# Performance work log

Measured on AMD Instinct MI355X. Metric: run time of the kernel, lower is better.

Reference implementation:

```python
import jax, jax.numpy as jnp
import numpy as np

L, D_MODEL, D_INNER, DT_RANK, D_STATE, D_CONV, VOCAB = 4, 768, 1536, 48, 16, 4, 32000
B, S = 1, 1024


def rmsnorm(x, w, eps=1e-5):
    return x * jax.lax.rsqrt(jnp.mean(x * x, axis=-1, keepdims=True) + eps) * w


def causal_depthwise_conv(x, w, b):
    # x: [B,S,D]; w: [D,1,K] (torch Conv1d groups=D weight layout); causal left-pad K-1
    y = jax.lax.conv_general_dilated(
        x.transpose(0, 2, 1), w, window_strides=(1,), padding=[(D_CONV - 1, 0)],
        dimension_numbers=('NCH', 'OIH', 'NCH'), feature_group_count=D_INNER)
    return y.transpose(0, 2, 1) + b


def selective_scan(u, dt, A, Bm, Cm, Dv):
    # Faithful to the source: A_delta = exp(dt (x) A), clamp(min=-20) is a no-op on exp output
    A_delta = jnp.clip(jnp.exp(jnp.einsum('bld,dn->bldn', dt, A)), -20.0, None)
    B_delta_u = jnp.einsum('bld,bld,bln->bldn', dt, u, Bm)
    shifted = jnp.pad(A_delta[:, 1:], ((0, 0), (1, 0), (0, 0), (0, 0)))
    A_cum = jnp.exp(jnp.cumsum(shifted, axis=1))
    h = B_delta_u / (A_cum + 1e-12)
    y = jnp.einsum('bldn,bln->bld', jnp.cumsum(h, axis=1) * A_cum, Cm)
    return y + u * Dv


def setup_inputs() -> dict:
    key = jax.random.key(0)
    ks = jax.random.split(key, 8)
    return {
        'tokens': jax.random.randint(ks[0], (B, S), 0, VOCAB),
        'embedding': jax.random.normal(ks[1], (VOCAB, D_MODEL), jnp.float32) * 0.02,
        'norm_w': jnp.ones((L, D_MODEL), jnp.float32),
        'in_proj_w': jax.random.normal(ks[2], (L, 2 * D_INNER, D_MODEL), jnp.float32) * 0.02,
        'conv_w': jax.random.normal(ks[3], (L, D_INNER, 1, D_CONV), jnp.float32) * 0.2,
        'conv_b': jnp.zeros((L, D_INNER), jnp.float32),
        'x_proj_w': jax.random.normal(ks[4], (L, DT_RANK + 2 * D_STATE, D_INNER), jnp.float32) * 0.02,
        'dt_proj_w': jax.random.normal(ks[5], (L, D_INNER, DT_RANK), jnp.float32) * 0.001,
        'dt_proj_b': jnp.full((L, D_INNER), 5.0, jnp.float32),  # delta~5 keeps exp(cumsum(exp(dt*A))) finite
        'A_log': jnp.tile(jnp.log(jnp.arange(1, D_STATE + 1, dtype=jnp.float32)), (L, D_INNER, 1)),
        'D_skip': jnp.ones((L, D_INNER), jnp.float32),
        'out_proj_w': jax.random.normal(ks[6], (L, D_MODEL, D_INNER), jnp.float32) * 0.02,
        'final_norm_w': jnp.ones((D_MODEL,), jnp.float32),
    }


def reference(tokens, embedding, norm_w, in_proj_w, conv_w, conv_b, x_proj_w,
              dt_proj_w, dt_proj_b, A_log, D_skip, out_proj_w, final_norm_w):
    x = embedding[tokens]  # [B,S,d_model]
    for i in range(L):
        h = rmsnorm(x, norm_w[i])
        xz = h @ in_proj_w[i].T                      # [B,S,2*d_inner]
        xi, res = xz[..., :D_INNER], xz[..., D_INNER:]
        xi = jax.nn.silu(causal_depthwise_conv(xi, conv_w[i], conv_b[i]))
        proj = xi @ x_proj_w[i].T                    # [B,S,dt_rank+2*d_state]
        dt = jax.nn.softplus(proj[..., :DT_RANK] @ dt_proj_w[i].T + dt_proj_b[i])
        Bm = proj[..., DT_RANK:DT_RANK + D_STATE]
        Cm = proj[..., DT_RANK + D_STATE:]
        A = -jnp.exp(A_log[i])                       # [d_inner, d_state]
        y = selective_scan(xi, dt, A, Bm, Cm, D_skip[i])
        x = x + (y * jax.nn.silu(res)) @ out_proj_w[i].T
    return rmsnorm(x, final_norm_w) @ embedding.T    # tied LM head: [B,S,vocab]
```

## Files before the change

kernel.cpp:

```cpp
#include <hip/hip_runtime.h>
#include <hip/hip_bf16.h>
#include <cmath>

namespace {

constexpr int kL      = 4;
constexpr int kDModel = 768;
constexpr int kDInner = 1536;
constexpr int kDtRank = 48;
constexpr int kDState = 16;
constexpr int kDConv  = 4;
constexpr int kSeq    = 1024;
constexpr int kPLd    = 96;
constexpr int kPB     = 128;
constexpr int kVocab  = 32000;
constexpr int kCH     = 64;
constexpr int kNCH    = kSeq / kCH;
constexpr int kDN     = kDInner * kDState;

using short8 = __attribute__((ext_vector_type(8))) short;
using f32x4  = __attribute__((ext_vector_type(4))) float;

__device__ __forceinline__ float silu_f(float v) {
    return v / (1.f + __expf(-v));
}

__device__ __forceinline__ void split_bf16(float v, __hip_bfloat16& hi, __hip_bfloat16& lo) {
    hi = __float2bfloat16(v);
    lo = __float2bfloat16(v - __bfloat162float(hi));
}

__global__ void __launch_bounds__(256) f2b_kernel(
    const float* __restrict__ src, __hip_bfloat16* __restrict__ dst, int n) {
    int i = (blockIdx.x * 256 + threadIdx.x) * 4;
    const int stride = gridDim.x * 256 * 4;
    for (; i + 3 < n; i += stride) {
        const float4 v = *reinterpret_cast<const float4*>(src + i);
        dst[i + 0] = __float2bfloat16(v.x);
        dst[i + 1] = __float2bfloat16(v.y);
        dst[i + 2] = __float2bfloat16(v.z);
        dst[i + 3] = __float2bfloat16(v.w);
    }
}

__global__ void __launch_bounds__(256) split3_kernel(
    const float* __restrict__ src, int ldsrc, int rows, int cols,
    __hip_bfloat16* __restrict__ dst, int rowsPad) {
    const int idx = blockIdx.x * 256 + threadIdx.x;
    if (idx >= rowsPad * cols) return;
    const int r = idx / cols, c = idx % cols;
    const float v = (r < rows) ? src[(size_t)r * ldsrc + c] : 0.f;
    __hip_bfloat16 hi, lo;
    split_bf16(v, hi, lo);
    __hip_bfloat16* row = dst + (size_t)r * 3 * cols;
    row[c] = hi; row[cols + c] = hi; row[2 * cols + c] = lo;
}

__global__ void __launch_bounds__(256) embed_kernel(
    const int* __restrict__ tokens, const float* __restrict__ emb,
    float* __restrict__ x) {
    const int s = blockIdx.x;
    const int t = tokens[s];
    const float* src = emb + (size_t)t * kDModel;
    float* dst = x + (size_t)s * kDModel;
    for (int d = threadIdx.x; d < kDModel; d += blockDim.x) dst[d] = src[d];
}

template <bool SPLIT>
__global__ void __launch_bounds__(256) rmsnorm_kernel(
    const float* __restrict__ x, const float* __restrict__ w,
    __hip_bfloat16* __restrict__ out) {
    const int s = blockIdx.x;
    const float* row = x + (size_t)s * kDModel;
    float ss = 0.f;
    for (int d = threadIdx.x; d < kDModel; d += blockDim.x) {
        const float v = row[d];
        ss = fmaf(v, v, ss);
    }
    #pragma unroll
    for (int m = 32; m; m >>= 1) ss += __shfl_xor(ss, m);
    __shared__ float red[4];
    if ((threadIdx.x & 63) == 0) red[threadIdx.x >> 6] = ss;
    __syncthreads();
    const float total = red[0] + red[1] + red[2] + red[3];
    const float scale = rsqrtf(total / (float)kDModel + 1e-5f);
    __hip_bfloat16* dst = out + (size_t)s * (SPLIT ? 3 * kDModel : kDModel);
    for (int d = threadIdx.x; d < kDModel; d += blockDim.x) {
        const float v = row[d] * scale * w[d];
        if (SPLIT) {
            __hip_bfloat16 hi, lo;
            split_bf16(v, hi, lo);
            dst[d] = hi; dst[kDModel + d] = lo; dst[2 * kDModel + d] = hi;
        } else {
            dst[d] = __float2bfloat16(v);
        }
    }
}

template <int BM, int BN, int KSPLIT>
__global__ void __launch_bounds__((BN == 256) ? 512 : 256) mfma_gemm(
    const __hip_bfloat16* __restrict__ A, int lda,
    const __hip_bfloat16* __restrict__ B, int ldb,
    float* __restrict__ C, int ldc,
    int N, int K, size_t partStride) {
    constexpr int BK = 32;
    constexpr int THREADS = (BN == 256) ? 512 : 256;
    constexpr int WAVES_M = 2;
    constexpr int WAVES_N = THREADS / 64 / WAVES_M;
    constexpr int LPT = (BM * 4 + BN * 4) / THREADS;
    static_assert(BM == 128, "A staging assumes BM=128");
    __shared__ unsigned short As[2][BM * BK];
    __shared__ unsigned short Bs[2][BN * BK];
    const int tid  = threadIdx.x;
    const int lane = tid & 63;

    const int nwg = gridDim.x * gridDim.y;
    int bid = blockIdx.y * gridDim.x + blockIdx.x;
    {
        const int q = nwg >> 3, r = nwg & 7;
        const int xcd = bid & 7, pos = bid >> 3;
        bid = (xcd < r ? xcd * (q + 1) : r * (q + 1) + (xcd - r) * q) + pos;
    }
    const int m0 = (bid % gridDim.x) * BM;
    const int n0 = (bid / gridDim.x) * BN;

    const int Kp = K / KSPLIT;
    const int kbeg = (KSPLIT > 1) ? blockIdx.z * Kp : 0;
    float* Cw = (KSPLIT > 1) ? C + (size_t)blockIdx.z * partStride : C;
    constexpr int WM = BM / WAVES_M, WN = BN / WAVES_N;
    constexpr int MR = WM / 16, NR = WN / 16;
    const int wave = tid >> 6;
    const int wm = (wave / WAVES_N) * WM, wn = (wave % WAVES_N) * WN;
    const int l15 = lane & 15, l4 = lane >> 4;
    f32x4 acc[MR][NR] = {};

    auto stage = [&](int buf, int k0) {
        #pragma unroll
        for (int i = 0; i < BM * 4 / THREADS; ++i) {
            const int idx = tid + i * THREADS;
            const int r = idx >> 2, qv = idx & 3;
            const int qs = qv ^ ((r >> 1) & 3);
            __builtin_amdgcn_global_load_lds(
                (const __attribute__((address_space(1))) void*)(A + (size_t)(m0 + r) * lda + k0 + qs * 8),
                (__attribute__((address_space(3))) void*)(&As[buf][(idx - lane) * 8]),
                16, 0, 0);
        }
        #pragma unroll
        for (int i = 0; i < BN * 4 / THREADS; ++i) {
            const int idx = tid + i * THREADS;
            const int r = idx >> 2, qv = idx & 3;
            const int qs = qv ^ ((r >> 1) & 3);
            __builtin_amdgcn_global_load_lds(
                (const __attribute__((address_space(1))) void*)(B + (size_t)(n0 + r) * ldb + k0 + qs * 8),
                (__attribute__((address_space(3))) void*)(&Bs[buf][(idx - lane) * 8]),
                16, 0, 0);
        }
    };

    const int nt = Kp / BK;
    int cur = 0;
    stage(0, kbeg);
    for (int t = 0; t < nt; ++t) {
        if (t + 1 < nt) {
            stage(cur ^ 1, kbeg + (t + 1) * BK);
            if constexpr (LPT == 4) asm volatile("s_waitcnt vmcnt(4)" ::: "memory");
            else                    asm volatile("s_waitcnt vmcnt(3)" ::: "memory");
        } else {
            asm volatile("s_waitcnt vmcnt(0)" ::: "memory");
        }
        __builtin_amdgcn_s_barrier();

        short8 af[MR], bfv[NR];
        #pragma unroll
        for (int mi = 0; mi < MR; ++mi) {
            const int R = wm + mi * 16 + l15;
            af[mi] = *reinterpret_cast<const short8*>(&As[cur][(R * 4 + (l4 ^ ((R >> 1) & 3))) * 8]);
        }
        #pragma unroll
        for (int ni = 0; ni < NR; ++ni) {
            const int R = wn + ni * 16 + l15;
            bfv[ni] = *reinterpret_cast<const short8*>(&Bs[cur][(R * 4 + (l4 ^ ((R >> 1) & 3))) * 8]);
        }
        #pragma unroll
        for (int mi = 0; mi < MR; ++mi)
            #pragma unroll
            for (int ni = 0; ni < NR; ++ni)
                acc[mi][ni] = __builtin_amdgcn_mfma_f32_16x16x32_bf16(
                    af[mi], bfv[ni], acc[mi][ni], 0, 0, 0);

        asm volatile("s_waitcnt lgkmcnt(0)" ::: "memory");
        __builtin_amdgcn_s_barrier();
        cur ^= 1;
    }

    #pragma unroll
    for (int mi = 0; mi < MR; ++mi) {
        const int mrow = m0 + wm + mi * 16 + l4 * 4;
        #pragma unroll
        for (int ni = 0; ni < NR; ++ni) {
            const int ncol = n0 + wn + ni * 16 + l15;
            if (ncol >= N) continue;
            #pragma unroll
            for (int r = 0; r < 4; ++r)
                Cw[(size_t)(mrow + r) * ldc + ncol] = acc[mi][ni][r];
        }
    }
}

template <int NP, bool ADD>
__global__ void __launch_bounds__(256) reduce_parts(
    const float* __restrict__ parts, size_t stride,
    float* __restrict__ dst, int count) {
    const int i = (blockIdx.x * 256 + threadIdx.x) * 4;
    if (i >= count) return;
    float4 s = *reinterpret_cast<const float4*>(parts + i);
    #pragma unroll
    for (int p = 1; p < NP; ++p) {
        const float4 v = *reinterpret_cast<const float4*>(parts + (size_t)p * stride + i);
        s.x += v.x; s.y += v.y; s.z += v.z; s.w += v.w;
    }
    float4* d = reinterpret_cast<float4*>(dst + i);
    if (ADD) {
        float4 o = *d;
        o.x += s.x; o.y += s.y; o.z += s.z; o.w += s.w;
        *d = o;
    } else {
        *d = s;
    }
}

__global__ void __launch_bounds__(256) dt_kernel(
    const float* __restrict__ proj, const float* __restrict__ dtw,
    const float* __restrict__ bias, float* __restrict__ dt) {
    __shared__ float sw[kDtRank][257];
    const int tid = threadIdx.x;
    const int n0 = blockIdx.x * 256;
    const int m0 = blockIdx.y * 8;
    for (int idx = tid; idx < 256 * kDtRank; idx += 256) {
        const int nn = idx / kDtRank, k = idx % kDtRank;
        sw[k][nn] = dtw[(size_t)(n0 + nn) * kDtRank + k];
    }
    __syncthreads();
    const int n = n0 + tid;
    const float b = bias[n];
    #pragma unroll
    for (int mi = 0; mi < 8; ++mi) {
        const float* pr = proj + (size_t)(m0 + mi) * kPLd;
        float acc = b;
        #pragma unroll
        for (int k = 0; k < kDtRank; ++k)
            acc = fmaf(pr[k], sw[k][tid], acc);
        acc = (acc > 20.f) ? acc : log1pf(__expf(acc));
        dt[(size_t)(m0 + mi) * kDInner + n] = acc;
    }
}

__global__ void __launch_bounds__(256) conv_silu_kernel(
    const float* __restrict__ p0, const float* __restrict__ p1,
    const float* __restrict__ cw, const float* __restrict__ cb,
    float* __restrict__ xi, __hip_bfloat16* __restrict__ xi2) {
    const int s = blockIdx.x;
    const int d = blockIdx.y * 256 + threadIdx.x;
    float acc = cb[d];
    #pragma unroll
    for (int k = 0; k < kDConv; ++k) {
        const int sl = s - (kDConv - 1) + k;
        if (sl >= 0) {
            const size_t off = (size_t)sl * (2 * kDInner) + d;
            acc = fmaf(p0[off] + p1[off], cw[d * kDConv + k], acc);
        }
    }
    const float v = silu_f(acc);
    xi[(size_t)s * kDInner + d] = v;
    __hip_bfloat16 hi, lo;
    split_bf16(v, hi, lo);
    __hip_bfloat16* row = xi2 + (size_t)s * 3 * kDInner;
    row[d] = hi; row[kDInner + d] = lo; row[2 * kDInner + d] = hi;
}

__global__ void __launch_bounds__(256) scan_part1(
    const float* __restrict__ dt, const float* __restrict__ u,
    const float* __restrict__ proj, const float* __restrict__ A_log,
    float* __restrict__ P, float* __restrict__ S) {
    __shared__ float sdt[kCH][16], su[kCH][16], sB[kCH][16];
    const int tid = threadIdx.x;
    const int n = tid & 15, dl = tid >> 4;
    const int d0 = blockIdx.x * 16;
    const int l0 = blockIdx.y * kCH;
    for (int idx = tid; idx < kCH * 16; idx += 256) {
        const int r = idx >> 4, c = idx & 15;
        sdt[r][c] = dt[(size_t)(l0 + r) * kDInner + d0 + c];
        su [r][c] = u [(size_t)(l0 + r) * kDInner + d0 + c];
        sB [r][c] = proj[(size_t)(l0 + r) * kPLd + kDtRank + c];
    }
    __syncthreads();
    const int d = d0 + dl;
    const float Adn = -__expf(A_log[d * kDState + n]);
    float state = 0.f, sumA = 0.f;
    #pragma unroll 8
    for (int l = 0; l < kCH; ++l) {
        const float dtv = sdt[l][dl];
        const float adelta = __expf(dtv * Adn);
        const float mult = __expf(adelta);
        state = fmaf(state, mult, dtv * su[l][dl] * sB[l][n]);
        sumA += adelta;
    }
    const int dn = d * kDState + n;
    P[(size_t)blockIdx.y * kDN + dn] = __expf(sumA);
    S[(size_t)blockIdx.y * kDN + dn] = state;
}

__global__ void __launch_bounds__(256) scan_part2(
    const float* __restrict__ dt, const float* __restrict__ u,
    const float* __restrict__ proj, const float* __restrict__ A_log,
    const float* __restrict__ D_skip, const float* __restrict__ P,
    const float* __restrict__ S, float* __restrict__ y) {
    __shared__ float sdt[kCH][16], su[kCH][16], sB[kCH][16], sC[kCH][16];
    __shared__ float sy[kCH][16];
    const int tid = threadIdx.x;
    const int n = tid & 15, dl = tid >> 4;
    const int d0 = blockIdx.x * 16;
    const int l0 = blockIdx.y * kCH;
    for (int idx = tid; idx < kCH * 16; idx += 256) {
        const int r = idx >> 4, c = idx & 15;
        sdt[r][c] = dt[(size_t)(l0 + r) * kDInner + d0 + c];
        su [r][c] = u [(size_t)(l0 + r) * kDInner + d0 + c];
        sB [r][c] = proj[(size_t)(l0 + r) * kPLd + kDtRank + c];
        sC [r][c] = proj[(size_t)(l0 + r) * kPLd + kDtRank + kDState + c];
    }
    const int dn = d0 * kDState + tid;
    float state = 0.f;
    for (int jj = 0; jj < (int)blockIdx.y; ++jj) {
        const size_t idx = (size_t)jj * kDN + dn;
        state = fmaf(state, P[idx], S[idx]);
    }
    __syncthreads();
    const int d = d0 + dl;
    const float Adn = -__expf(A_log[d * kDState + n]);
    const float Dv  = D_skip[d];
    for (int l = 0; l < kCH; ++l) {
        const float dtv = sdt[l][dl];
        const float uv  = su[l][dl];
        const float mult = __expf(__expf(dtv * Adn));
        state = fmaf(state, mult, dtv * uv * sB[l][n]);
        float contrib = state * sC[l][n];
        contrib += __shfl_xor(contrib, 8);
        contrib += __shfl_xor(contrib, 4);
        contrib += __shfl_xor(contrib, 2);
        contrib += __shfl_xor(contrib, 1);
        if (n == 0) sy[l][dl] = fmaf(uv, Dv, contrib);
    }
    __syncthreads();
    for (int idx = tid; idx < kCH * 16; idx += 256) {
        const int r = idx >> 4, c = idx & 15;
        y[(size_t)(l0 + r) * kDInner + d0 + c] = sy[r][c];
    }
}

__global__ void __launch_bounds__(256) mul_silu_kernel(
    const float* __restrict__ y, const float* __restrict__ p0,
    const float* __restrict__ p1, __hip_bfloat16* __restrict__ g2) {
    const int s = blockIdx.x;
    const int d = blockIdx.y * 256 + threadIdx.x;
    const size_t off = (size_t)s * (2 * kDInner) + kDInner + d;
    const float res = p0[off] + p1[off];
    const float v = y[(size_t)s * kDInner + d] * silu_f(res);
    __hip_bfloat16 hi, lo;
    split_bf16(v, hi, lo);
    __hip_bfloat16* row = g2 + (size_t)s * 3 * kDInner;
    row[d] = hi; row[kDInner + d] = lo; row[2 * kDInner + d] = hi;
}

}

extern "C" void kernel_launch(void* const* d_in, const int* in_sizes, int n_in,
                              void* d_out, int out_size, void* d_ws, size_t ws_size,
                              hipStream_t stream) {
    const int*   tokens       = (const int*)d_in[0];
    const float* embedding    = (const float*)d_in[1];
    const float* norm_w       = (const float*)d_in[2];
    const float* in_proj_w    = (const float*)d_in[3];
    const float* conv_w       = (const float*)d_in[4];
    const float* conv_b       = (const float*)d_in[5];
    const float* x_proj_w     = (const float*)d_in[6];
    const float* dt_proj_w    = (const float*)d_in[7];
    const float* dt_proj_b    = (const float*)d_in[8];
    const float* A_log        = (const float*)d_in[9];
    const float* D_skip       = (const float*)d_in[10];
    const float* out_proj_w   = (const float*)d_in[11];
    const float* final_norm_w = (const float*)d_in[12];
    float* out = (float*)d_out;

    constexpr int K3m = 3 * kDModel;
    constexpr int K3i = 3 * kDInner;

    char* ws = (char*)d_ws;
    auto alloc = [&](size_t bytes) { char* p = ws; ws += (bytes + 255) & ~(size_t)255; return p; };
    float* x    = (float*)alloc((size_t)kSeq * kDModel * 4);
    float* xi   = (float*)alloc((size_t)kSeq * kDInner * 4);
    float* proj = (float*)alloc((size_t)kSeq * kPLd * 4);
    float* dt   = (float*)alloc((size_t)kSeq * kDInner * 4);
    float* y    = (float*)alloc((size_t)kSeq * kDInner * 4);
    float* scanP  = (float*)alloc((size_t)kNCH * kDN * 4);
    float* scanS  = (float*)alloc((size_t)kNCH * kDN * 4);
    float* partsXZ = (float*)alloc((size_t)2 * kSeq * 2 * kDInner * 4);
    float* partsP  = (float*)alloc((size_t)24 * kSeq * kPLd * 4);
    float* partsO  = (float*)alloc((size_t)6 * kSeq * kDModel * 4);
    __hip_bfloat16* h_bf   = (__hip_bfloat16*)alloc((size_t)kSeq * kDModel * 2);
    __hip_bfloat16* h2     = (__hip_bfloat16*)alloc((size_t)kSeq * K3m * 2);
    __hip_bfloat16* xi2    = (__hip_bfloat16*)alloc((size_t)kSeq * K3i * 2);
    __hip_bfloat16* g2     = (__hip_bfloat16*)alloc((size_t)kSeq * K3i * 2);
    __hip_bfloat16* emb_bf = (__hip_bfloat16*)alloc((size_t)kVocab * kDModel * 2);
    __hip_bfloat16* inw2   = (__hip_bfloat16*)alloc((size_t)kL * 2 * kDInner * K3m * 2);
    __hip_bfloat16* outw2  = (__hip_bfloat16*)alloc((size_t)kL * kDModel * K3i * 2);
    __hip_bfloat16* xw2    = (__hip_bfloat16*)alloc((size_t)kL * kPB * K3i * 2);

    f2b_kernel<<<4096, 256, 0, stream>>>(embedding, emb_bf, kVocab * kDModel);
    split3_kernel<<<(kL * 2 * kDInner * kDModel + 255) / 256, 256, 0, stream>>>(
        in_proj_w, kDModel, kL * 2 * kDInner, kDModel, inw2, kL * 2 * kDInner);
    split3_kernel<<<(kL * kDModel * kDInner + 255) / 256, 256, 0, stream>>>(
        out_proj_w, kDInner, kL * kDModel, kDInner, outw2, kL * kDModel);
    for (int i = 0; i < kL; ++i)
        split3_kernel<<<(kPB * kDInner + 255) / 256, 256, 0, stream>>>(
            x_proj_w + (size_t)i * (kDtRank + 2 * kDState) * kDInner, kDInner,
            kDtRank + 2 * kDState, kDInner, xw2 + (size_t)i * kPB * K3i, kPB);

    embed_kernel<<<kSeq, 256, 0, stream>>>(tokens, embedding, x);

    for (int i = 0; i < kL; ++i) {
        rmsnorm_kernel<true><<<kSeq, 256, 0, stream>>>(x, norm_w + (size_t)i * kDModel, h2);

        mfma_gemm<128, 128, 2><<<dim3(kSeq / 128, 2 * kDInner / 128, 2), 256, 0, stream>>>(
            h2, K3m, inw2 + (size_t)i * 2 * kDInner * K3m, K3m,
            partsXZ, 2 * kDInner, 2 * kDInner, K3m, (size_t)kSeq * 2 * kDInner);

        conv_silu_kernel<<<dim3(kSeq, kDInner / 256), 256, 0, stream>>>(
            partsXZ, partsXZ + (size_t)kSeq * 2 * kDInner,
            conv_w + (size_t)i * kDInner * kDConv, conv_b + (size_t)i * kDInner,
            xi, xi2);

        mfma_gemm<128, 128, 24><<<dim3(kSeq / 128, 1, 24), 256, 0, stream>>>(
            xi2, K3i, xw2 + (size_t)i * kPB * K3i, K3i,
            partsP, kPLd, kPLd, K3i, (size_t)kSeq * kPLd);
        reduce_parts<24, false><<<(kSeq * kPLd / 4 + 255) / 256, 256, 0, stream>>>(
            partsP, (size_t)kSeq * kPLd, proj, kSeq * kPLd);

        dt_kernel<<<dim3(kDInner / 256, kSeq / 8), 256, 0, stream>>>(
            proj, dt_proj_w + (size_t)i * kDInner * kDtRank,
            dt_proj_b + (size_t)i * kDInner, dt);

        const float* A_l = A_log + (size_t)i * kDInner * kDState;
        scan_part1<<<dim3(kDInner / 16, kNCH), 256, 0, stream>>>(
            dt, xi, proj, A_l, scanP, scanS);
        scan_part2<<<dim3(kDInner / 16, kNCH), 256, 0, stream>>>(
            dt, xi, proj, A_l, D_skip + (size_t)i * kDInner, scanP, scanS, y);

        mul_silu_kernel<<<dim3(kSeq, kDInner / 256), 256, 0, stream>>>(
            y, partsXZ, partsXZ + (size_t)kSeq * 2 * kDInner, g2);

        mfma_gemm<128, 128, 6><<<dim3(kSeq / 128, kDModel / 128, 6), 256, 0, stream>>>(
            g2, K3i, outw2 + (size_t)i * kDModel * K3i, K3i,
            partsO, kDModel, kDModel, K3i, (size_t)kSeq * kDModel);
        reduce_parts<6, true><<<(kSeq * kDModel / 4 + 255) / 256, 256, 0, stream>>>(
            partsO, (size_t)kSeq * kDModel, x, kSeq * kDModel);
    }

    rmsnorm_kernel<false><<<kSeq, 256, 0, stream>>>(x, final_norm_w, h_bf);
    mfma_gemm<128, 256, 1><<<dim3(kSeq / 128, kVocab / 256, 1), 512, 0, stream>>>(
        h_bf, kDModel, emb_bf, kDModel, out, kVocab, kVocab, kDModel, 0);
}
```

Baseline: 822.5 us.

## Triple-buffer GEMM LDS staging and use 128x128 tiles for LM head

The MFMA GEMM moves from double to triple buffering. Tiles are prefetched two steps ahead, with vmcnt waits set to match, so more global-to-LDS loads are in flight while the MFMAs run. The kernel is specialised to 128x128 tiles with 256 threads, and the LM-head GEMM switches from 128x256 tiles with 512 threads to 128x128 tiles with 256 threads. The four per-layer x_proj weight split launches are merged into one. The third buffer raises LDS use per block, which may lower occupancy, and the smaller LM-head tile reloads the A operand more often.

```diff
diff --git a/kernel.cpp b/kernel.cpp
--- a/kernel.cpp
+++ b/kernel.cpp
@@ -54,6 +54,22 @@
     split_bf16(v, hi, lo);
     __hip_bfloat16* row = dst + (size_t)r * 3 * cols;
     row[c] = hi; row[cols + c] = hi; row[2 * cols + c] = lo;
+}
+
+__global__ void __launch_bounds__(256) split3x_kernel(
+    const float* __restrict__ src, __hip_bfloat16* __restrict__ dst) {
+    const int idx = blockIdx.x * 256 + threadIdx.x;
+    if (idx >= kL * kPB * kDInner) return;
+    const int layer = idx / (kPB * kDInner);
+    const int rem   = idx % (kPB * kDInner);
+    const int r = rem / kDInner, c = rem % kDInner;
+    const float v = (r < kDtRank + 2 * kDState)
+        ? src[(size_t)layer * (kDtRank + 2 * kDState) * kDInner + (size_t)r * kDInner + c]
+        : 0.f;
+    __hip_bfloat16 hi, lo;
+    split_bf16(v, hi, lo);
+    __hip_bfloat16* row = dst + ((size_t)layer * kPB + r) * 3 * kDInner;
+    row[c] = hi; row[kDInner + c] = hi; row[2 * kDInner + c] = lo;
 }
 
 __global__ void __launch_bounds__(256) embed_kernel(
@@ -98,19 +114,15 @@
 }
 
 template <int BM, int BN, int KSPLIT>
-__global__ void __launch_bounds__((BN == 256) ? 512 : 256) mfma_gemm(
+__global__ void __launch_bounds__(256) mfma_gemm(
     const __hip_bfloat16* __restrict__ A, int lda,
     const __hip_bfloat16* __restrict__ B, int ldb,
     float* __restrict__ C, int ldc,
     int N, int K, size_t partStride) {
     constexpr int BK = 32;
-    constexpr int THREADS = (BN == 256) ? 512 : 256;
-    constexpr int WAVES_M = 2;
-    constexpr int WAVES_N = THREADS / 64 / WAVES_M;
-    constexpr int LPT = (BM * 4 + BN * 4) / THREADS;
-    static_assert(BM == 128, "A staging assumes BM=128");
-    __shared__ unsigned short As[2][BM * BK];
-    __shared__ unsigned short Bs[2][BN * BK];
+    static_assert(BM == 128 && BN == 128, "staging assumes 128x128");
+    __shared__ unsigned short As[3][BM * BK];
+    __shared__ unsigned short Bs[3][BN * BK];
     const int tid  = threadIdx.x;
     const int lane = tid & 63;
 
@@ -127,17 +139,17 @@
     const int Kp = K / KSPLIT;
     const int kbeg = (KSPLIT > 1) ? blockIdx.z * Kp : 0;
     float* Cw = (KSPLIT > 1) ? C + (size_t)blockIdx.z * partStride : C;
-    constexpr int WM = BM / WAVES_M, WN = BN / WAVES_N;
+    constexpr int WM = BM / 2, WN = BN / 2;
     constexpr int MR = WM / 16, NR = WN / 16;
     const int wave = tid >> 6;
-    const int wm = (wave / WAVES_N) * WM, wn = (wave % WAVES_N) * WN;
+    const int wm = (wave >> 1) * WM, wn = (wave & 1) * WN;
     const int l15 = lane & 15, l4 = lane >> 4;
     f32x4 acc[MR][NR] = {};
 
     auto stage = [&](int buf, int k0) {
         #pragma unroll
-        for (int i = 0; i < BM * 4 / THREADS; ++i) {
-            const int idx = tid + i * THREADS;
+        for (int i = 0; i < 2; ++i) {
+            const int idx = tid + i * 256;
             const int r = idx >> 2, qv = idx & 3;
             const int qs = qv ^ ((r >> 1) & 3);
             __builtin_amdgcn_global_load_lds(
@@ -146,8 +158,8 @@
                 16, 0, 0);
         }
         #pragma unroll
-        for (int i = 0; i < BN * 4 / THREADS; ++i) {
-            const int idx = tid + i * THREADS;
+        for (int i = 0; i < 2; ++i) {
+            const int idx = tid + i * 256;
             const int r = idx >> 2, qv = idx & 3;
             const int qs = qv ^ ((r >> 1) & 3);
             __builtin_amdgcn_global_load_lds(
@@ -158,16 +170,15 @@
     };
 
     const int nt = Kp / BK;
-    int cur = 0;
     stage(0, kbeg);
+    if (nt > 1) stage(1, kbeg + BK);
     for (int t = 0; t < nt; ++t) {
-        if (t + 1 < nt) {
-            stage(cur ^ 1, kbeg + (t + 1) * BK);
-            if constexpr (LPT == 4) asm volatile("s_waitcnt vmcnt(4)" ::: "memory");
-            else                    asm volatile("s_waitcnt vmcnt(3)" ::: "memory");
-        } else {
-            asm volatile("s_waitcnt vmcnt(0)" ::: "memory");
-        }
+        const int cur = t % 3;
+        if (t + 2 < nt) stage((t + 2) % 3, kbeg + (t + 2) * BK);
+        const int rem = nt - 1 - t;
+        if (rem >= 2)      asm volatile("s_waitcnt vmcnt(8)" ::: "memory");
+        else if (rem == 1) asm volatile("s_waitcnt vmcnt(4)" ::: "memory");
+        else               asm volatile("s_waitcnt vmcnt(0)" ::: "memory");
         __builtin_amdgcn_s_barrier();
 
         short8 af[MR], bfv[NR];
@@ -190,7 +201,6 @@
 
         asm volatile("s_waitcnt lgkmcnt(0)" ::: "memory");
         __builtin_amdgcn_s_barrier();
-        cur ^= 1;
     }
 
     #pragma unroll
@@ -420,10 +430,8 @@
         in_proj_w, kDModel, kL * 2 * kDInner, kDModel, inw2, kL * 2 * kDInner);
     split3_kernel<<<(kL * kDModel * kDInner + 255) / 256, 256, 0, stream>>>(
         out_proj_w, kDInner, kL * kDModel, kDInner, outw2, kL * kDModel);
-    for (int i = 0; i < kL; ++i)
-        split3_kernel<<<(kPB * kDInner + 255) / 256, 256, 0, stream>>>(
-            x_proj_w + (size_t)i * (kDtRank + 2 * kDState) * kDInner, kDInner,
-            kDtRank + 2 * kDState, kDInner, xw2 + (size_t)i * kPB * K3i, kPB);
+    split3x_kernel<<<(kL * kPB * kDInner + 255) / 256, 256, 0, stream>>>(
+        x_proj_w, xw2);
 
     embed_kernel<<<kSeq, 256, 0, stream>>>(tokens, embedding, x);
 
@@ -466,6 +474,6 @@
     }
 
     rmsnorm_kernel<false><<<kSeq, 256, 0, stream>>>(x, final_norm_w, h_bf);
-    mfma_gemm<128, 256, 1><<<dim3(kSeq / 128, kVocab / 256, 1), 512, 0, stream>>>(
+    mfma_gemm<128, 128, 1><<<dim3(kSeq / 128, kVocab / 128, 1), 256, 0, stream>>>(
         h_bf, kDModel, emb_bf, kDModel, out, kVocab, kVocab, kDModel, 0);
 }
```

Result: no change. 819.7 us (-0.3%).
